# Kernel optimization log

Hardware: AMD Instinct MI355X
Metric: run time of the kernel (lower is better)

Reference implementation:

```python
import jax, jax.numpy as jnp
import numpy as np

B, T, C = 1, 2048, 1024
H, KVH = 16, 4
D = C // H            # 64
KV = KVH * D          # 256
EPS = 1e-6
SCALE = 1.0 / np.sqrt(D)
ROPE_BASE = 10000.0


def setup_inputs() -> dict:
    key = jax.random.key(0)
    ks = jax.random.split(key, 8)
    s = 0.02
    return dict(
        x=jax.random.normal(ks[0], (B, T, C), jnp.float32),
        Wq=jax.random.normal(ks[1], (C, C), jnp.float32) * s,
        Wk=jax.random.normal(ks[2], (KV, C), jnp.float32) * s,
        Wv=jax.random.normal(ks[3], (KV, C), jnp.float32) * s,
        Wo=jax.random.normal(ks[4], (C, C), jnp.float32) * s,
        q_norm_w=jnp.ones((C,), jnp.float32),
        k_norm_w=jnp.ones((KV,), jnp.float32),
        fgate_w=jax.random.normal(ks[5], (H, C), jnp.float32) * s,
        fgate_b=jnp.zeros((H,), jnp.float32),
        weight_lambda=jax.random.normal(ks[6], (C, H), jnp.float32) * s,
    )


def _rmsnorm(x, w):
    var = jnp.mean(x * x, axis=-1, keepdims=True)
    return x * jax.lax.rsqrt(var + EPS) * w


def _rotate_half(x):
    x1, x2 = jnp.split(x, 2, axis=-1)
    return jnp.concatenate([-x2, x1], axis=-1)


def _apply_rope(q, k):
    # q: [B,H,T,D], k: [B,KVH,T,D]; position_ids = arange(T)
    inv_freq = 1.0 / (ROPE_BASE ** (jnp.arange(0, D, 2, dtype=jnp.float32) / D))
    freqs = jnp.outer(jnp.arange(T, dtype=jnp.float32), inv_freq)  # [T, D/2]
    emb = jnp.concatenate([freqs, freqs], axis=-1)                 # [T, D]
    cos = jnp.cos(emb)[None, None]                                  # [1,1,T,D]
    sin = jnp.sin(emb)[None, None]
    return q * cos + _rotate_half(q) * sin, k * cos + _rotate_half(k) * sin


def _forward(x, Wq, Wk, Wv, Wo, q_norm_w, k_norm_w, fgate_w, fgate_b, weight_lambda):
    q = _rmsnorm(x @ Wq.T, q_norm_w)          # [B,T,C]
    k = _rmsnorm(x @ Wk.T, k_norm_w)          # [B,T,KV]
    v = x @ Wv.T                              # [B,T,KV]
    q = q.reshape(B, T, H, D).transpose(0, 2, 1, 3)     # [B,H,T,D]
    k = k.reshape(B, T, KVH, D).transpose(0, 2, 1, 3)   # [B,KVH,T,D]
    v = v.reshape(B, T, KVH, D).transpose(0, 2, 1, 3)
    q, k = _apply_rope(q, k)
    # GQA: repeat_interleave kv heads
    g = H // KVH
    k = jnp.repeat(k, g, axis=1)              # [B,H,T,D]
    v = jnp.repeat(v, g, axis=1)
    # Forgetting gate (FoX): log f_t per head, with elu-based lambda scaling
    lam = jax.nn.elu(x @ weight_lambda) + 1.0            # [B,T,H]
    logit = (x @ fgate_w.T + fgate_b) * lam              # [B,T,H]
    log_f = (jax.nn.log_sigmoid(logit) / (lam + 1e-3)).transpose(0, 2, 1)  # [B,H,T]
    c = jnp.cumsum(log_f, axis=-1)                       # [B,H,T]
    bias = c[..., :, None] - c[..., None, :]             # [B,H,T,T]: sum_{t=j+1..i} log f_t
    scores = jnp.einsum('bhid,bhjd->bhij', q, k) * SCALE + bias
    causal = jnp.tril(jnp.ones((T, T), dtype=bool))
    scores = jnp.where(causal, scores, -jnp.inf)
    p = jax.nn.softmax(scores, axis=-1)
    y = jnp.einsum('bhij,bhjd->bhid', p, v)              # [B,H,T,D]
    y = y.transpose(0, 2, 1, 3).reshape(B, T, C)
    return y @ Wo.T


def reference(x, Wq, Wk, Wv, Wo, q_norm_w, k_norm_w, fgate_w, fgate_b, weight_lambda):
    return _forward(x, Wq, Wk, Wv, Wo, q_norm_w, k_norm_w, fgate_w, fgate_b, weight_lambda)
```

## Files before the change

### kernel.cpp

```cpp
#include <hip/hip_runtime.h>

typedef __bf16 bf16x8 __attribute__((ext_vector_type(8)));
typedef float f32x4 __attribute__((ext_vector_type(4)));

#define MFMA_BF16 __builtin_amdgcn_mfma_f32_16x16x32_bf16

static constexpr int T_ = 2048;
static constexpr int C_ = 1024;
static constexpr int H_ = 16;
static constexpr int KVH_ = 4;
static constexpr int D_ = 64;
static constexpr float SCALE_ = 0.125f;
static constexpr float MSHIFT_ = 10.0f;

static constexpr int UPH_ = 528;
static constexpr int W_ = H_ * UPH_;
static constexpr int CHUNK_ = 3;
static constexpr int NBLK_ = W_ / CHUNK_;

__device__ inline void cvt8(__bf16* dst, const float* src) {
  float4 a = *(const float4*)src;
  float4 b = *(const float4*)(src + 4);
  bf16x8 r;
  r[0] = (__bf16)a.x; r[1] = (__bf16)a.y; r[2] = (__bf16)a.z; r[3] = (__bf16)a.w;
  r[4] = (__bf16)b.x; r[5] = (__bf16)b.y; r[6] = (__bf16)b.z; r[7] = (__bf16)b.w;
  *(bf16x8*)dst = r;
}

__global__ __launch_bounds__(256) void cvt_kernel(
    const float* __restrict__ x,  const float* __restrict__ wq,
    const float* __restrict__ wk, const float* __restrict__ wv,
    const float* __restrict__ wo, const float* __restrict__ wl,
    __bf16* __restrict__ xb,  __bf16* __restrict__ wqb,
    __bf16* __restrict__ wkb, __bf16* __restrict__ wvb,
    __bf16* __restrict__ wob, float* __restrict__ wlT,
    float* __restrict__ zbuf)
{
  size_t i8 = ((size_t)blockIdx.x * 256 + threadIdx.x) * 8;
  if (i8 < 2097152)       cvt8(xb  + i8,            x  + i8);
  else if (i8 < 3145728)  cvt8(wqb + (i8-2097152),  wq + (i8-2097152));
  else if (i8 < 3407872)  cvt8(wkb + (i8-3145728),  wk + (i8-3145728));
  else if (i8 < 3670016)  cvt8(wvb + (i8-3407872),  wv + (i8-3407872));
  else if (i8 < 4718592)  cvt8(wob + (i8-3670016),  wo + (i8-3670016));
  else if (i8 < 4734976) {
    size_t r = i8 - 4718592;
#pragma unroll
    for (int j = 0; j < 8; ++j) {
      size_t idx = r + j;
      size_t hh = idx >> 10, c = idx & 1023;
      wlT[idx] = wl[c * 16 + hh];
    }
  } else {
    size_t z = i8 - 4734976;
    if (z < 2129920) {
      float4 zz = {0.f, 0.f, 0.f, 0.f};
      *(float4*)(zbuf + z) = zz;
      *(float4*)(zbuf + z + 4) = zz;
    }
  }
}

template <int BM>
__global__ __launch_bounds__(256) void gemm_bt_kernel(
    const __bf16* __restrict__ A, int K, int N,
    const __bf16* __restrict__ B0, int e0,
    const __bf16* __restrict__ B1, int e1,
    const __bf16* __restrict__ B2,
    float* __restrict__ outF)
{
  __shared__ __bf16 la[BM * 40];
  __shared__ __bf16 lb[128 * 40];
  const int m0 = blockIdx.y * BM;
  const int n0 = blockIdx.x * 128;
  const __bf16* Bs; int nrel;
  if (n0 < e0)      { Bs = B0; nrel = n0; }
  else if (n0 < e1) { Bs = B1; nrel = n0 - e0; }
  else              { Bs = B2; nrel = n0 - e1; }
  const int tid = threadIdx.x;
  const int arow = tid >> 2, acol = (tid & 3) * 8;
  const __bf16* ap = A  + (size_t)(m0   + arow) * K + acol;
  const __bf16* bp = Bs + (size_t)(nrel + arow) * K + acol;
  const int w = tid >> 6, lane = tid & 63, lq = lane >> 4, ln = lane & 15;
  const int wm = (w >> 1) * (BM / 2), wn = (w & 1) * 64;
  constexpr int FM = BM / 32;
  f32x4 acc[FM][4] = {};
  for (int k0 = 0; k0 < K; k0 += 32) {
    bf16x8 a0 = *(const bf16x8*)(ap + k0);
    bf16x8 a1{};
    if (BM == 128) a1 = *(const bf16x8*)(ap + (size_t)64 * K + k0);
    bf16x8 b0 = *(const bf16x8*)(bp + k0);
    bf16x8 b1 = *(const bf16x8*)(bp + (size_t)64 * K + k0);
    __syncthreads();
    *(bf16x8*)(la + arow * 40 + acol) = a0;
    if (BM == 128) *(bf16x8*)(la + (arow + 64) * 40 + acol) = a1;
    *(bf16x8*)(lb + arow * 40 + acol) = b0;
    *(bf16x8*)(lb + (arow + 64) * 40 + acol) = b1;
    __syncthreads();
    bf16x8 af[FM], bfr[4];
#pragma unroll
    for (int i = 0; i < FM; ++i)
      af[i] = *(const bf16x8*)(la + (wm + i * 16 + ln) * 40 + lq * 8);
#pragma unroll
    for (int j = 0; j < 4; ++j)
      bfr[j] = *(const bf16x8*)(lb + (wn + j * 16 + ln) * 40 + lq * 8);
#pragma unroll
    for (int i = 0; i < FM; ++i)
#pragma unroll
      for (int j = 0; j < 4; ++j)
        acc[i][j] = MFMA_BF16(af[i], bfr[j], acc[i][j], 0, 0, 0);
  }
#pragma unroll
  for (int i = 0; i < FM; ++i)
#pragma unroll
    for (int j = 0; j < 4; ++j)
#pragma unroll
      for (int r = 0; r < 4; ++r) {
        int row = m0 + wm + i * 16 + lq * 4 + r;
        int col = n0 + wn + j * 16 + ln;
        outF[(size_t)row * N + col] = acc[i][j][r];
      }
}

__global__ __launch_bounds__(256) void gates_kernel(
    const float* __restrict__ x, const float* __restrict__ fw,
    const float* __restrict__ fb, const float* __restrict__ wlT,
    float* __restrict__ logf)
{
  const int t = blockIdx.x;
  const int tid = threadIdx.x, w = tid >> 6, lane = tid & 63;
  float xv[16];
#pragma unroll
  for (int i = 0; i < 16; ++i)
    xv[i] = x[(size_t)t * C_ + i * 64 + lane];
#pragma unroll
  for (int u = 0; u < 4; ++u) {
    int h = w * 4 + u;
    float s1 = 0.f, s2 = 0.f;
#pragma unroll
    for (int i = 0; i < 16; ++i) {
      int cidx = i * 64 + lane;
      s1 += xv[i] * wlT[(size_t)h * C_ + cidx];
      s2 += xv[i] * fw[(size_t)h * C_ + cidx];
    }
    for (int m = 32; m; m >>= 1) {
      s1 += __shfl_xor(s1, m);
      s2 += __shfl_xor(s2, m);
    }
    if (lane == 0) {
      float lam = (s1 > 0.f ? s1 : expm1f(s1)) + 1.0f;
      float logit = (s2 + fb[h]) * lam;
      float ls = (logit >= 0.f) ? -log1pf(expf(-logit))
                                : (logit - log1pf(expf(logit)));
      logf[(size_t)h * T_ + t] = ls / (lam + 1e-3f);
    }
  }
}

__global__ __launch_bounds__(64) void cumsum_kernel(
    const float* __restrict__ logf, float* __restrict__ csum)
{
  const int h = blockIdx.x;
  const int lane = threadIdx.x;
  float carry = 0.f;
  for (int ch = 0; ch < T_ / 64; ++ch) {
    float v = logf[(size_t)h * T_ + ch * 64 + lane];
#pragma unroll
    for (int d = 1; d < 64; d <<= 1) {
      float tv = __shfl_up(v, d);
      if (lane >= d) v += tv;
    }
    v += carry;
    csum[(size_t)h * T_ + ch * 64 + lane] = v;
    carry = __shfl(v, 63);
  }
}

__global__ __launch_bounds__(256) void normrope_kernel(
    const float* __restrict__ qkv, const float* __restrict__ qw,
    const float* __restrict__ kw, __bf16* __restrict__ qh,
    __bf16* __restrict__ kh, __bf16* __restrict__ vh)
{
  const int t = blockIdx.x, tid = threadIdx.x;
  __shared__ float qn[1024];
  __shared__ float kn[256];
  __shared__ float red[16];
  __shared__ float rc[32], rs[32];
  if (tid < 32) {
    float fr = (float)t * exp2f((float)tid * -0.41524101186404527f);
    float sn, cs;
    sincosf(fr, &sn, &cs);
    rc[tid] = cs; rs[tid] = sn;
  }
  const float* row = qkv + (size_t)t * 1536;
  float4 q4 = *(const float4*)(row + tid * 4);
  float kvl = row[1024 + tid];
  float vvl = row[1280 + tid];
  float ssq = q4.x * q4.x + q4.y * q4.y + q4.z * q4.z + q4.w * q4.w;
  float ssk = kvl * kvl;
  const int lane = tid & 63, w = tid >> 6;
  for (int m = 32; m; m >>= 1) {
    ssq += __shfl_xor(ssq, m);
    ssk += __shfl_xor(ssk, m);
  }
  if (lane == 0) { red[w] = ssq; red[8 + w] = ssk; }
  __syncthreads();
  float sq = red[0] + red[1] + red[2] + red[3];
  float sk = red[8] + red[9] + red[10] + red[11];
  float rq = rsqrtf(sq * (1.0f / 1024.f) + 1e-6f);
  float rk = rsqrtf(sk * (1.0f / 256.f) + 1e-6f);
  qn[tid * 4 + 0] = q4.x * rq * qw[tid * 4 + 0];
  qn[tid * 4 + 1] = q4.y * rq * qw[tid * 4 + 1];
  qn[tid * 4 + 2] = q4.z * rq * qw[tid * 4 + 2];
  qn[tid * 4 + 3] = q4.w * rq * qw[tid * 4 + 3];
  kn[tid] = kvl * rk * kw[tid];
  __syncthreads();
#pragma unroll
  for (int u = 0; u < 4; ++u) {
    int cidx = tid * 4 + u;
    int hh = cidx >> 6, d = cidx & 63, i = d & 31;
    float cs = rc[i], sn = rs[i];
    float val = (d < 32) ? (qn[cidx] * cs - qn[cidx + 32] * sn)
                         : (qn[cidx] * cs + qn[cidx - 32] * sn);
    qh[(size_t)hh * T_ * D_ + (size_t)t * D_ + d] = (__bf16)val;
  }
  {
    int d = tid & 63, kvhh = tid >> 6, i = d & 31;
    float cs = rc[i], sn = rs[i];
    float kval = (d < 32) ? (kn[tid] * cs - kn[tid + 32] * sn)
                          : (kn[tid] * cs + kn[tid - 32] * sn);
    kh[(size_t)kvhh * T_ * D_ + (size_t)t * D_ + d] = (__bf16)kval;
    vh[(size_t)kvhh * T_ * D_ + (size_t)t * D_ + d] = (__bf16)vvl;
  }
}

__global__ __launch_bounds__(256) void vtrans_kernel(
    const __bf16* __restrict__ vh, __bf16* __restrict__ vt)
{
  const int tb = blockIdx.x, kvh = blockIdx.y;
  __shared__ __bf16 tile[64][72];
  const int tid = threadIdx.x;
  const int r = tid >> 2, cb = (tid & 3) * 16;
  const __bf16* src = vh + (size_t)kvh * T_ * D_ + (size_t)(tb * 64 + r) * D_ + cb;
  bf16x8 v0 = *(const bf16x8*)(src);
  bf16x8 v1 = *(const bf16x8*)(src + 8);
  *(bf16x8*)(&tile[r][cb]) = v0;
  *(bf16x8*)(&tile[r][cb + 8]) = v1;
  __syncthreads();
  bf16x8 o0, o1;
#pragma unroll
  for (int j = 0; j < 8; ++j) o0[j] = tile[cb + j][r];
#pragma unroll
  for (int j = 0; j < 8; ++j) o1[j] = tile[cb + 8 + j][r];
  __bf16* dst = vt + (size_t)kvh * D_ * T_ + (size_t)r * T_ + tb * 64 + cb;
  *(bf16x8*)(dst) = o0;
  *(bf16x8*)(dst + 8) = o1;
}

__global__ __launch_bounds__(256, 5) void attn_kernel(
    const __bf16* __restrict__ qh, const __bf16* __restrict__ kh,
    const __bf16* __restrict__ vt, const float* __restrict__ csum,
    float* __restrict__ oacc, float* __restrict__ lsacc)
{
  const int bid = blockIdx.x;
  const int wgid = (bid & 7) * (NBLK_ / 8) + (bid >> 3);
  const int u0 = wgid * CHUNK_;
  __shared__ __bf16 kt[64 * 72];
  __shared__ __bf16 vtt[64 * 72];
  __shared__ __bf16 pt[4][16 * 76];
  const int tid = threadIdx.x;
  const int w = tid >> 6, lane = tid & 63, lq = lane >> 4, ln = lane & 15;
  const int srow = tid >> 2, scol = (tid & 3) * 16;
  bf16x8 ones;
#pragma unroll
  for (int j = 0; j < 8; ++j) ones[j] = (__bf16)1.0f;
  __bf16* pw = &pt[w][0];

  auto dec = [](int u, int& h, int& ib, int& jt) {
    h = u / UPH_;
    int uh = u - h * UPH_;
    int b = (int)((sqrtf((float)(8 * uh + 1)) - 1.f) * 0.5f);
    if (b * (b + 1) / 2 > uh) --b;
    if ((b + 1) * (b + 2) / 2 <= uh) ++b;
    ib = b; jt = uh - b * (b + 1) / 2;
  };

  int h, ib, jt;
  dec(u0, h, ib, jt);
  int kvh = h >> 2;

  bf16x8 aq0, aq1;
  float ci[4];
  f32x4 o[4] = {};
  f32x4 ls = {0.f, 0.f, 0.f, 0.f};
  auto loadQ = [&](int h_, int i0_) {
    const __bf16* qp = qh + ((size_t)h_ * T_ + i0_ + w * 16 + ln) * D_;
    aq0 = *(const bf16x8*)(qp + lq * 8);
    aq1 = *(const bf16x8*)(qp + 32 + lq * 8);
#pragma unroll
    for (int r = 0; r < 4; ++r)
      ci[r] = csum[(size_t)h_ * T_ + i0_ + w * 16 + lq * 4 + r];
#pragma unroll
    for (int dd = 0; dd < 4; ++dd) o[dd] = f32x4{0.f, 0.f, 0.f, 0.f};
    ls = f32x4{0.f, 0.f, 0.f, 0.f};
  };
  loadQ(h, ib * 64);

  auto fetchRegs = [&](int kvh_, int jt_, bf16x8& k0, bf16x8& k1,
                       bf16x8& v0, bf16x8& v1) {
    const __bf16* kb = kh + (size_t)kvh_ * T_ * D_;
    const __bf16* vb = vt + (size_t)kvh_ * D_ * T_;
    k0 = *(const bf16x8*)(kb + (size_t)(jt_ * 64 + srow) * D_ + scol);
    k1 = *(const bf16x8*)(kb + (size_t)(jt_ * 64 + srow) * D_ + scol + 8);
    v0 = *(const bf16x8*)(vb + (size_t)srow * T_ + jt_ * 64 + scol);
    v1 = *(const bf16x8*)(vb + (size_t)srow * T_ + jt_ * 64 + scol + 8);
  };
  auto writeStage = [&](bf16x8 k0, bf16x8 k1, bf16x8 v0, bf16x8 v1) {
    *(bf16x8*)(kt + srow * 72 + scol) = k0;
    *(bf16x8*)(kt + srow * 72 + scol + 8) = k1;
    *(bf16x8*)(vtt + srow * 72 + scol) = v0;
    *(bf16x8*)(vtt + srow * 72 + scol + 8) = v1;
  };

  auto tilebody = [&](int j0, bool diag) {
    float cj[4];
#pragma unroll
    for (int jj = 0; jj < 4; ++jj)
      cj[jj] = csum[(size_t)h * T_ + j0 + jj * 16 + ln];
    f32x4 s[4];
    const f32x4 zf = {0.f, 0.f, 0.f, 0.f};
#pragma unroll
    for (int jj = 0; jj < 4; ++jj) {
      bf16x8 bk0 = *(const bf16x8*)(kt + (jj * 16 + ln) * 72 + lq * 8);
      bf16x8 bk1 = *(const bf16x8*)(kt + (jj * 16 + ln) * 72 + 32 + lq * 8);
      s[jj] = MFMA_BF16(aq0, bk0, zf, 0, 0, 0);
      s[jj] = MFMA_BF16(aq1, bk1, s[jj], 0, 0, 0);
    }
#pragma unroll
    for (int jj = 0; jj < 4; ++jj)
#pragma unroll
      for (int r = 0; r < 4; ++r) {
        float arg = fmaf(s[jj][r], SCALE_, ci[r] - cj[jj] - MSHIFT_);
        float p = __expf(arg);
        if (diag && (jj * 16 + ln > w * 16 + lq * 4 + r)) p = 0.f;
        pw[(lq * 4 + r) * 76 + jj * 16 + ln] = (__bf16)p;
      }
    asm volatile("s_waitcnt lgkmcnt(0)" ::: "memory");
    bf16x8 pa0 = *(const bf16x8*)(pw + ln * 76 + lq * 8);
    bf16x8 pa1 = *(const bf16x8*)(pw + ln * 76 + 32 + lq * 8);
    ls = MFMA_BF16(pa0, ones, ls, 0, 0, 0);
    ls = MFMA_BF16(pa1, ones, ls, 0, 0, 0);
#pragma unroll
    for (int dd = 0; dd < 4; ++dd) {
      bf16x8 bv0 = *(const bf16x8*)(vtt + (dd * 16 + ln) * 72 + lq * 8);
      bf16x8 bv1 = *(const bf16x8*)(vtt + (dd * 16 + ln) * 72 + 32 + lq * 8);
      o[dd] = MFMA_BF16(pa0, bv0, o[dd], 0, 0, 0);
      o[dd] = MFMA_BF16(pa1, bv1, o[dd], 0, 0, 0);
    }
  };

  auto flush = [&]() {
    const int i0 = ib * 64;
#pragma unroll
    for (int dd = 0; dd < 4; ++dd)
#pragma unroll
      for (int r = 0; r < 4; ++r) {
        int iabs = i0 + w * 16 + lq * 4 + r;
        atomicAdd(oacc + ((size_t)h * T_ + iabs) * D_ + dd * 16 + ln,
                  o[dd][r]);
      }
    if (ln == 0) {
#pragma unroll
      for (int r = 0; r < 4; ++r)
        atomicAdd(lsacc + (size_t)h * T_ + ib * 64 + w * 16 + lq * 4 + r,
                  ls[r]);
    }
  };

  {
    bf16x8 k0, k1, v0, v1;
    fetchRegs(kvh, jt, k0, k1, v0, v1);
    writeStage(k0, k1, v0, v1);
  }
  __syncthreads();

#pragma unroll
  for (int s = 0; s < CHUNK_; ++s) {
    const bool last = (s == CHUNK_ - 1);
    int nh = 0, nib = 0, njt = 0;
    bf16x8 k0, k1, v0, v1;
    if (!last) {
      dec(u0 + s + 1, nh, nib, njt);
      fetchRegs(nh >> 2, njt, k0, k1, v0, v1);
    }
    tilebody(jt * 64, jt == ib);
    const bool rowEnd = last || nib != ib || nh != h;
    if (rowEnd) flush();
    if (!last) {
      __syncthreads();
      writeStage(k0, k1, v0, v1);
      __syncthreads();
      if (nh != h || nib != ib) loadQ(nh, nib * 64);
      h = nh; ib = nib; jt = njt; kvh = nh >> 2;
    }
  }
}

__global__ __launch_bounds__(256) void attnfin_kernel(
    const float* __restrict__ oacc, const float* __restrict__ lsacc,
    __bf16* __restrict__ y)
{
  const int t = blockIdx.x;
  const int c = threadIdx.x * 4;
  const int h = c >> 6, d = c & 63;
  float inv = 1.0f / lsacc[(size_t)h * T_ + t];
  float4 o4 = *(const float4*)(oacc + ((size_t)h * T_ + t) * D_ + d);
  __bf16* yp = y + (size_t)t * C_ + c;
  yp[0] = (__bf16)(o4.x * inv);
  yp[1] = (__bf16)(o4.y * inv);
  yp[2] = (__bf16)(o4.z * inv);
  yp[3] = (__bf16)(o4.w * inv);
}

extern "C" void kernel_launch(void* const* d_in, const int* in_sizes, int n_in,
                              void* d_out, int out_size, void* d_ws, size_t ws_size,
                              hipStream_t stream) {
  const float* x   = (const float*)d_in[0];
  const float* Wq  = (const float*)d_in[1];
  const float* Wk  = (const float*)d_in[2];
  const float* Wv  = (const float*)d_in[3];
  const float* Wo  = (const float*)d_in[4];
  const float* qnw = (const float*)d_in[5];
  const float* knw = (const float*)d_in[6];
  const float* fgw = (const float*)d_in[7];
  const float* fgb = (const float*)d_in[8];
  const float* wl  = (const float*)d_in[9];

  char* ws = (char*)d_ws;
  size_t off = 0;
  float*  qkv  = (float*)(ws + off);  off += (size_t)T_ * 1536 * 4;
  float*  logf = (float*)(ws + off);  off += (size_t)H_ * T_ * 4;
  float*  csum = (float*)(ws + off);  off += (size_t)H_ * T_ * 4;
  __bf16* qh   = (__bf16*)(ws + off); off += (size_t)H_ * T_ * D_ * 2;
  __bf16* kh   = (__bf16*)(ws + off); off += (size_t)KVH_ * T_ * D_ * 2;
  __bf16* vh   = (__bf16*)(ws + off); off += (size_t)KVH_ * T_ * D_ * 2;
  __bf16* vt   = (__bf16*)(ws + off); off += (size_t)KVH_ * T_ * D_ * 2;
  __bf16* y    = (__bf16*)(ws + off); off += (size_t)T_ * C_ * 2;
  __bf16* xb   = (__bf16*)(ws + off); off += (size_t)T_ * C_ * 2;
  __bf16* wqb  = (__bf16*)(ws + off); off += (size_t)C_ * C_ * 2;
  __bf16* wkb  = (__bf16*)(ws + off); off += (size_t)256 * C_ * 2;
  __bf16* wvb  = (__bf16*)(ws + off); off += (size_t)256 * C_ * 2;
  __bf16* wob  = (__bf16*)(ws + off); off += (size_t)C_ * C_ * 2;
  float*  wlT  = (float*)(ws + off);  off += (size_t)H_ * C_ * 4;
  float*  oacc = (float*)(ws + off);  off += (size_t)H_ * T_ * D_ * 4;
  float*  lsacc= (float*)(ws + off);  off += (size_t)H_ * T_ * 4;

  cvt_kernel<<<3352, 256, 0, stream>>>(x, Wq, Wk, Wv, Wo, wl,
                                       xb, wqb, wkb, wvb, wob, wlT, oacc);
  gemm_bt_kernel<64><<<dim3(12, 32), 256, 0, stream>>>(
      xb, 1024, 1536, wqb, 1024, wkb, 1280, wvb, qkv);
  gates_kernel<<<T_, 256, 0, stream>>>(x, fgw, fgb, wlT, logf);
  cumsum_kernel<<<H_, 64, 0, stream>>>(logf, csum);
  normrope_kernel<<<T_, 256, 0, stream>>>(qkv, qnw, knw, qh, kh, vh);
  vtrans_kernel<<<dim3(T_ / 64, KVH_), 256, 0, stream>>>(vh, vt);
  attn_kernel<<<NBLK_, 256, 0, stream>>>(qh, kh, vt, csum, oacc, lsacc);
  attnfin_kernel<<<T_, 256, 0, stream>>>(oacc, lsacc, y);
  gemm_bt_kernel<64><<<dim3(8, 32), 256, 0, stream>>>(
      y, 1024, 1024, wob, 1024, wob, 1024, wob, (float*)d_out);
}
```

Measured before the change: 217.9 us.

## Double-buffer K/V shared tiles and lengthen per-block work chunks

The single K/V LDS stage becomes a two-slot ring. The next tile is written into the alternate slot right after the current tile is computed, which removes one of the two barriers per iteration. The V-fragment loads are hoisted ahead of the softmax exponentials, the chunk of work units per block grows from 3 to 12 (fewer blocks, fewer atomic flushes), the loop is no longer unrolled, and the occupancy hint in the launch bounds is dropped. In exchange, LDS use doubles and there are fewer blocks to balance the load.

```diff
diff --git a/kernel.cpp b/kernel.cpp
--- a/kernel.cpp
+++ b/kernel.cpp
@@ -15,7 +15,7 @@
 
 static constexpr int UPH_ = 528;
 static constexpr int W_ = H_ * UPH_;
-static constexpr int CHUNK_ = 3;
+static constexpr int CHUNK_ = 12;
 static constexpr int NBLK_ = W_ / CHUNK_;
 
 __device__ inline void cvt8(__bf16* dst, const float* src) {
@@ -256,7 +256,7 @@
   *(bf16x8*)(dst + 8) = o1;
 }
 
-__global__ __launch_bounds__(256, 5) void attn_kernel(
+__global__ __launch_bounds__(256) void attn_kernel(
     const __bf16* __restrict__ qh, const __bf16* __restrict__ kh,
     const __bf16* __restrict__ vt, const float* __restrict__ csum,
     float* __restrict__ oacc, float* __restrict__ lsacc)
@@ -264,8 +264,8 @@
   const int bid = blockIdx.x;
   const int wgid = (bid & 7) * (NBLK_ / 8) + (bid >> 3);
   const int u0 = wgid * CHUNK_;
-  __shared__ __bf16 kt[64 * 72];
-  __shared__ __bf16 vtt[64 * 72];
+  __shared__ __bf16 kbuf[2][64 * 72];
+  __shared__ __bf16 vbuf[2][64 * 72];
   __shared__ __bf16 pt[4][16 * 76];
   const int tid = threadIdx.x;
   const int w = tid >> 6, lane = tid & 63, lq = lane >> 4, ln = lane & 15;
@@ -314,14 +314,16 @@
     v0 = *(const bf16x8*)(vb + (size_t)srow * T_ + jt_ * 64 + scol);
     v1 = *(const bf16x8*)(vb + (size_t)srow * T_ + jt_ * 64 + scol + 8);
   };
-  auto writeStage = [&](bf16x8 k0, bf16x8 k1, bf16x8 v0, bf16x8 v1) {
-    *(bf16x8*)(kt + srow * 72 + scol) = k0;
-    *(bf16x8*)(kt + srow * 72 + scol + 8) = k1;
-    *(bf16x8*)(vtt + srow * 72 + scol) = v0;
-    *(bf16x8*)(vtt + srow * 72 + scol + 8) = v1;
-  };
-
-  auto tilebody = [&](int j0, bool diag) {
+  auto writeStage = [&](int cb, bf16x8 k0, bf16x8 k1, bf16x8 v0, bf16x8 v1) {
+    *(bf16x8*)(kbuf[cb] + srow * 72 + scol) = k0;
+    *(bf16x8*)(kbuf[cb] + srow * 72 + scol + 8) = k1;
+    *(bf16x8*)(vbuf[cb] + srow * 72 + scol) = v0;
+    *(bf16x8*)(vbuf[cb] + srow * 72 + scol + 8) = v1;
+  };
+
+  auto tilebody = [&](int cb, int j0, bool diag) {
+    const __bf16* kt = kbuf[cb];
+    const __bf16* vtt = vbuf[cb];
     float cj[4];
 #pragma unroll
     for (int jj = 0; jj < 4; ++jj)
@@ -334,6 +336,12 @@
       bf16x8 bk1 = *(const bf16x8*)(kt + (jj * 16 + ln) * 72 + 32 + lq * 8);
       s[jj] = MFMA_BF16(aq0, bk0, zf, 0, 0, 0);
       s[jj] = MFMA_BF16(aq1, bk1, s[jj], 0, 0, 0);
+    }
+    bf16x8 bv0[4], bv1[4];
+#pragma unroll
+    for (int dd = 0; dd < 4; ++dd) {
+      bv0[dd] = *(const bf16x8*)(vtt + (dd * 16 + ln) * 72 + lq * 8);
+      bv1[dd] = *(const bf16x8*)(vtt + (dd * 16 + ln) * 72 + 32 + lq * 8);
     }
 #pragma unroll
     for (int jj = 0; jj < 4; ++jj)
@@ -351,10 +359,8 @@
     ls = MFMA_BF16(pa1, ones, ls, 0, 0, 0);
 #pragma unroll
     for (int dd = 0; dd < 4; ++dd) {
-      bf16x8 bv0 = *(const bf16x8*)(vtt + (dd * 16 + ln) * 72 + lq * 8);
-      bf16x8 bv1 = *(const bf16x8*)(vtt + (dd * 16 + ln) * 72 + 32 + lq * 8);
-      o[dd] = MFMA_BF16(pa0, bv0, o[dd], 0, 0, 0);
-      o[dd] = MFMA_BF16(pa1, bv1, o[dd], 0, 0, 0);
+      o[dd] = MFMA_BF16(pa0, bv0[dd], o[dd], 0, 0, 0);
+      o[dd] = MFMA_BF16(pa1, bv1[dd], o[dd], 0, 0, 0);
     }
   };
 
@@ -379,11 +385,12 @@
   {
     bf16x8 k0, k1, v0, v1;
     fetchRegs(kvh, jt, k0, k1, v0, v1);
-    writeStage(k0, k1, v0, v1);
+    writeStage(0, k0, k1, v0, v1);
   }
   __syncthreads();
 
-#pragma unroll
+  int cur = 0;
+#pragma unroll 1
   for (int s = 0; s < CHUNK_; ++s) {
     const bool last = (s == CHUNK_ - 1);
     int nh = 0, nib = 0, njt = 0;
@@ -392,15 +399,15 @@
       dec(u0 + s + 1, nh, nib, njt);
       fetchRegs(nh >> 2, njt, k0, k1, v0, v1);
     }
-    tilebody(jt * 64, jt == ib);
+    tilebody(cur, jt * 64, jt == ib);
+    if (!last) writeStage(cur ^ 1, k0, k1, v0, v1);
     const bool rowEnd = last || nib != ib || nh != h;
     if (rowEnd) flush();
     if (!last) {
       __syncthreads();
-      writeStage(k0, k1, v0, v1);
-      __syncthreads();
       if (nh != h || nib != ib) loadQ(nh, nib * 64);
       h = nh; ib = nib; jt = njt; kvh = nh >> 2;
+      cur ^= 1;
     }
   }
 }
```

Result: faster. 197.3 us (-9.5%).
